# Optimization experiments

Measured on AMD Instinct MI355X. Metric: run time of the kernel, lower is better.

The kernel has to match this reference:

```python
import jax, jax.numpy as jnp
import numpy as np

NUM_ORI = 16
DEGREE = 2
NUM_LAYERS = 2
LN_EPS = 1e-6


def ori_grid_s1(n):
    theta = jnp.linspace(0.0, 2.0 * jnp.pi, n + 1)[:-1]
    return jnp.stack([jnp.cos(theta), jnp.sin(theta)], axis=-1)  # (O, 2)


def poly_feats(z, degree):
    # PolynomialFeatures: [z, z*z outer, (z*z)*z outer ...] flattened
    feats = [z]
    p = z
    for _ in range(degree):
        p = (p[..., :, None] * z[..., None, :]).reshape(*z.shape[:-1], -1)
        feats.append(p)
    return jnp.concatenate(feats, axis=-1)


def basis_mlp(z, W1, b1, W2, b2):
    return jax.nn.gelu(jax.nn.gelu(z @ W1 + b1) @ W2 + b2)


def layer_norm(h, scale, bias):
    mu = h.mean(axis=-1, keepdims=True)
    var = ((h - mu) ** 2).mean(axis=-1, keepdims=True)
    return (h - mu) * jax.lax.rsqrt(var + LN_EPS) * scale + bias


def setup_inputs() -> dict:
    key = jax.random.key(0)
    ks = jax.random.split(key, 16)
    B, N, NIN, H, BD, WF, OUT, L = 1, 256, 3, 64, 32, 4, 3, NUM_LAYERS
    s = 0.05
    return {
        'pos': jax.random.normal(ks[0], (B, N, 2), jnp.float32),
        'x': jax.random.normal(ks[1], (B, N, NIN), jnp.float32),
        'skb_W1': jax.random.normal(ks[2], (14, H), jnp.float32) * s,
        'skb_b1': jnp.zeros((H,), jnp.float32),
        'skb_W2': jax.random.normal(ks[3], (H, BD), jnp.float32) * s,
        'skb_b2': jnp.zeros((BD,), jnp.float32),
        'rkb_W1': jax.random.normal(ks[4], (3, H), jnp.float32) * s,
        'rkb_b1': jnp.zeros((H,), jnp.float32),
        'rkb_W2': jax.random.normal(ks[5], (H, BD), jnp.float32) * s,
        'rkb_b2': jnp.zeros((BD,), jnp.float32),
        'emb_W': jax.random.normal(ks[6], (NIN, H), jnp.float32) * s,
        'conv_sW': jax.random.normal(ks[7], (L, BD, H), jnp.float32) * s,
        'conv_rW': jax.random.normal(ks[8], (L, BD, H), jnp.float32) * s,
        'conv_b': jnp.zeros((L, H), jnp.float32),
        'ln_scale': jnp.ones((L, H), jnp.float32),
        'ln_bias': jnp.zeros((L, H), jnp.float32),
        'lin1_W': jax.random.normal(ks[9], (L, H, WF * H), jnp.float32) * s,
        'lin1_b': jnp.zeros((L, WF * H), jnp.float32),
        'lin2_W': jax.random.normal(ks[10], (L, WF * H, H), jnp.float32) * s,
        'lin2_b': jnp.zeros((L, H), jnp.float32),
        'readout_W': jax.random.normal(ks[11], (H, OUT), jnp.float32) * s,
    }


def reference(pos, x, skb_W1, skb_b1, skb_W2, skb_b2, rkb_W1, rkb_b1, rkb_W2, rkb_b2,
              emb_W, conv_sW, conv_rW, conv_b, ln_scale, ln_bias,
              lin1_W, lin1_b, lin2_W, lin2_b, readout_W):
    ori = ori_grid_s1(NUM_ORI)  # (O, 2)
    # rel_pos: (B, n, m, 1, 2) -> broadcast against ori (O, 2)
    rel_pos = pos[:, None, :, None, :] - pos[:, :, None, None, :]
    inv1 = jnp.sum(rel_pos * ori[None, None, None, :, :], axis=-1, keepdims=True)  # (B,N,N,O,1)
    inv2 = jnp.linalg.norm(rel_pos - rel_pos * inv1, axis=-1, keepdims=True)       # (B,N,N,O,1)
    spatial_inv = jnp.concatenate([inv1, inv2], axis=-1)                            # (B,N,N,O,2)
    orient_inv = jnp.sum(ori[:, None, :] * ori[None, :, :], axis=-1, keepdims=True) # (O,O,1)

    kernel_basis = basis_mlp(poly_feats(spatial_inv, DEGREE), skb_W1, skb_b1, skb_W2, skb_b2)  # (B,N,N,O,BD)
    fiber_basis = basis_mlp(poly_feats(orient_inv, DEGREE), rkb_W1, rkb_b1, rkb_W2, rkb_b2)    # (O,O,BD)

    h = x @ emb_W                                  # (B,N,H)
    O = NUM_ORI
    h = jnp.broadcast_to(h[:, :, None, :], (h.shape[0], h.shape[1], O, h.shape[2]))  # (B,N,O,H)

    for i in range(NUM_LAYERS):
        inp = h
        sk = kernel_basis @ conv_sW[i]             # (B,N,N,O,H)
        rk = fiber_basis @ conv_rW[i]              # (O,O,H)
        c = jnp.einsum('bnoc,bmnoc->bmoc', h, sk)  # spatial aggregation
        c = jnp.einsum('bmoc,poc->bmpc', c, rk)    # orientation mixing
        c = c + conv_b[i]
        c = layer_norm(c, ln_scale[i], ln_bias[i])
        c = jax.nn.gelu(c @ lin1_W[i] + lin1_b[i]) @ lin2_W[i] + lin2_b[i]
        h = inp + c

    readout = h @ readout_W                        # (B,N,O,OUT)
    out_scalar = readout.mean(axis=-2)             # (B,N,OUT)
    out_scalar = jnp.sum(out_scalar, axis=1) / out_scalar.shape[1]  # global pool -> (B,OUT)
    return out_scalar
```

## Files before the change

### kernel.cpp

```cpp
#include <hip/hip_runtime.h>
#include <math.h>

#define NPTS 256
#define NORI 16
#define CH   64
#define BD   32
#define HID  64
#define STEP16 0.39269908169872414f

typedef __bf16 bf16x8 __attribute__((ext_vector_type(8)));
typedef float  f32x4  __attribute__((ext_vector_type(4)));

#define MFMA16(a, b, cc) __builtin_amdgcn_mfma_f32_16x16x32_bf16(a, b, cc, 0, 0, 0)
#define GLOAD_LDS16(g, l) \
    __builtin_amdgcn_global_load_lds((const __attribute__((address_space(1))) unsigned int*)(g), \
                                     (__attribute__((address_space(3))) unsigned int*)(l), 16, 0, 0)

__device__ __forceinline__ float gelu_f(float x) {
    float x2 = x * x;
    float y2 = x * fmaf(0.07135481627f, x2, 1.5957691216f);
    float e = __expf(y2);
    return x - x * __builtin_amdgcn_rcpf(e + 1.0f);
}

__device__ __forceinline__ unsigned pk2(float x, float y) {
    union { __bf16 h[2]; unsigned u; } r;
    r.h[0] = (__bf16)x; r.h[1] = (__bf16)y;
    return r.u;
}

__device__ __forceinline__ void dev_prep(
    const float* __restrict__ skb_W1, const float* __restrict__ skb_W2,
    const float* __restrict__ conv_sW,
    __bf16* __restrict__ w1T, __bf16* __restrict__ w2T, __bf16* __restrict__ w2Tlo,
    __bf16* __restrict__ sWT, __bf16* __restrict__ sWTlo, int t)
{
    if (t < 64) {
        float f[9];
        f[0] = skb_W1[t];
        f[1] = skb_W1[64 + t];
        f[2] = skb_W1[128 + t];
        f[3] = skb_W1[192 + t] + skb_W1[256 + t];
        f[4] = skb_W1[320 + t];
        f[5] = skb_W1[384 + t];
        f[6] = skb_W1[448 + t] + skb_W1[512 + t] + skb_W1[640 + t];
        f[7] = skb_W1[576 + t] + skb_W1[704 + t] + skb_W1[768 + t];
        f[8] = skb_W1[832 + t];
#pragma unroll
        for (int k = 0; k < 9; ++k) {
            __bf16 hi = (__bf16)f[k];
            w1T[t * 32 + k]      = hi;
            w1T[t * 32 + 9 + k]  = (__bf16)(f[k] - (float)hi);
            w1T[t * 32 + 18 + k] = hi;
        }
#pragma unroll
        for (int k = 27; k < 32; ++k) w1T[t * 32 + k] = (__bf16)0.0f;
    }
    for (int i = t; i < 2048; i += 256) {
        int n = i >> 6, kk = i & 63;
        float v = skb_W2[kk * 32 + n];
        __bf16 hi = (__bf16)v;
        w2T[i]   = hi;
        w2Tlo[i] = (__bf16)(v - (float)hi);
    }
    for (int i = t; i < 4096; i += 256) {
        int ll = i >> 11, chh = (i >> 5) & 63, k = i & 31;
        float v = conv_sW[(ll * 32 + k) * 64 + chh];
        __bf16 hi = (__bf16)v;
        sWT[i]   = hi;
        sWTlo[i] = (__bf16)(v - (float)hi);
    }
}

__device__ __forceinline__ void dev_fiber(
    const float* __restrict__ rkb_W1, const float* __restrict__ rkb_b1,
    const float* __restrict__ rkb_W2, const float* __restrict__ rkb_b2,
    const float* __restrict__ conv_rW, float* __restrict__ rk, int p, int t)
{
    __shared__ float w1L[3 * 64], b1L[64], w2L[64 * 32], b2L[32];
    __shared__ float rwL[2 * 32 * 64];
    __shared__ float t1L[16 * 64];
    __shared__ float fbL[16 * 32];

    if (t < 192) w1L[t] = rkb_W1[t];
    if (t >= 192 && t < 256) b1L[t - 192] = rkb_b1[t - 192];
    for (int i = t; i < 2048; i += 256) w2L[i] = rkb_W2[i];
    if (t < 32) b2L[t] = rkb_b2[t];
    for (int i = t; i < 4096; i += 256) rwL[i] = conv_rW[i];
    __syncthreads();

    const int o = t & 15;
    const float cp = cosf(p * STEP16), sp = sinf(p * STEP16);
    const float co = cosf(o * STEP16), so = sinf(o * STEP16);
    const float s0 = cp * co + sp * so;
    const float m1 = s0 * s0, m2 = m1 * s0;

    {
        const int jg = t >> 4;
#pragma unroll
        for (int u = 0; u < 4; ++u) {
            const int j = jg * 4 + u;
            float a = b1L[j] + s0 * w1L[j] + m1 * w1L[64 + j] + m2 * w1L[128 + j];
            t1L[o * 64 + j] = gelu_f(a);
        }
    }
    __syncthreads();
    {
        const int kg = t >> 4;
#pragma unroll
        for (int kk = 0; kk < 2; ++kk) {
            const int k = kg + kk * 16;
            float a = b2L[k];
#pragma unroll
            for (int j = 0; j < 64; ++j) a += t1L[o * 64 + j] * w2L[j * 32 + k];
            fbL[o * 32 + k] = gelu_f(a);
        }
    }
    __syncthreads();
    {
        const int o2 = t >> 4;
        const int chg = (t & 15) * 4;
#pragma unroll
        for (int l = 0; l < 2; ++l) {
            f32x4 acc = {0.f, 0.f, 0.f, 0.f};
#pragma unroll
            for (int k = 0; k < 32; ++k) {
                const float fv = fbL[o2 * 32 + k];
                const f32x4 rv = *(const f32x4*)(rwL + (l * 32 + k) * 64 + chg);
                acc[0] = fmaf(fv, rv[0], acc[0]);
                acc[1] = fmaf(fv, rv[1], acc[1]);
                acc[2] = fmaf(fv, rv[2], acc[2]);
                acc[3] = fmaf(fv, rv[3], acc[3]);
            }
            *(f32x4*)(rk + (l * 256 + p * 16 + o2) * 64 + chg) = acc;
        }
    }
}

__global__ __launch_bounds__(256) void k_prep(
    const float* __restrict__ skb_W1, const float* __restrict__ skb_W2,
    const float* __restrict__ conv_sW,
    __bf16* __restrict__ w1T, __bf16* __restrict__ w2T, __bf16* __restrict__ w2Tlo,
    __bf16* __restrict__ sWT, __bf16* __restrict__ sWTlo)
{
    dev_prep(skb_W1, skb_W2, conv_sW, w1T, w2T, w2Tlo, sWT, sWTlo, threadIdx.x);
}

__global__ __launch_bounds__(256) void k_fiber2(
    const float* __restrict__ rkb_W1, const float* __restrict__ rkb_b1,
    const float* __restrict__ rkb_W2, const float* __restrict__ rkb_b2,
    const float* __restrict__ conv_rW, float* __restrict__ rk)
{
    dev_fiber(rkb_W1, rkb_b1, rkb_W2, rkb_b2, conv_rW, rk, blockIdx.x, threadIdx.x);
}

__global__ __launch_bounds__(256) void k_init(
    const float* __restrict__ x, const float* __restrict__ emb_W, float* __restrict__ h)
{
    int idx = blockIdx.x * 256 + threadIdx.x;
    int ch = idx & 63;
    int n  = idx >> 10;
    h[idx] = x[n * 3] * emb_W[ch] + x[n * 3 + 1] * emb_W[64 + ch] + x[n * 3 + 2] * emb_W[128 + ch];
}

__global__ __launch_bounds__(256) void k_setup(
    const float* __restrict__ x, const float* __restrict__ emb_W, float* __restrict__ h2,
    const float* __restrict__ rkb_W1, const float* __restrict__ rkb_b1,
    const float* __restrict__ rkb_W2, const float* __restrict__ rkb_b2,
    const float* __restrict__ conv_rW, float* __restrict__ rk,
    const float* __restrict__ skb_W1, const float* __restrict__ skb_W2,
    const float* __restrict__ conv_sW,
    __bf16* __restrict__ w1T, __bf16* __restrict__ w2T, __bf16* __restrict__ w2Tlo,
    __bf16* __restrict__ sWT, __bf16* __restrict__ sWTlo)
{
    const int b = blockIdx.x, t = threadIdx.x;
    if (b < 1024) {
        int idx = b * 256 + t;
        int ch = (idx >> 4) & 63;
        int n  = idx >> 10;
        h2[idx] = x[n * 3] * emb_W[ch] + x[n * 3 + 1] * emb_W[64 + ch]
                + x[n * 3 + 2] * emb_W[128 + ch];
    } else if (b < 1040) {
        dev_fiber(rkb_W1, rkb_b1, rkb_W2, rkb_b2, conv_rW, rk, b - 1024, t);
    } else {
        dev_prep(skb_W1, skb_W2, conv_sW, w1T, w2T, w2Tlo, sWT, sWTlo, t);
    }
}

__global__ __launch_bounds__(256) void k_kb2(
    const float* __restrict__ pos,
    const float* __restrict__ skb_b1, const float* __restrict__ skb_b2,
    const __bf16* __restrict__ w1T, const __bf16* __restrict__ w2T,
    const __bf16* __restrict__ w2Tlo, __bf16* __restrict__ kb_g)
{
    const int t = threadIdx.x;
    const int c = t & 15, qq = (t >> 4) & 3, w = t >> 6;
    const int b = blockIdx.x;
    const int pair = b >> 2;
    const int ohalf = (b >> 1) & 1;
    const int mhalf = b & 1;
    const int m0 = (pair >> 4) * 16, n0 = (pair & 15) * 16;

    bf16x8 w1B[4], w2A[2][2], w2Alo[2][2];
    float b1x[4][4], b2x[2][4];
#pragma unroll
    for (int ni = 0; ni < 4; ++ni) {
        w1B[ni] = *(const bf16x8*)(w1T + (ni * 16 + c) * 32 + qq * 8);
#pragma unroll
        for (int r = 0; r < 4; ++r) b1x[ni][r] = skb_b1[ni * 16 + qq * 4 + r];
    }
#pragma unroll
    for (int mk = 0; mk < 2; ++mk) {
#pragma unroll
        for (int ks = 0; ks < 2; ++ks) {
            w2A[mk][ks]   = *(const bf16x8*)(w2T   + (mk * 16 + c) * 64 + ks * 32 + qq * 8);
            w2Alo[mk][ks] = *(const bf16x8*)(w2Tlo + (mk * 16 + c) * 64 + ks * 32 + qq * 8);
        }
#pragma unroll
        for (int r = 0; r < 4; ++r) b2x[mk][r] = skb_b2[mk * 16 + qq * 4 + r];
    }

    const int n = n0 + c;
    const float pnx = pos[2 * n], pny = pos[2 * n + 1];
    float cosv[4], sinv[4];
#pragma unroll
    for (int oi = 0; oi < 4; ++oi) {
        float th = (float)(ohalf * 4 + oi) * STEP16;
        cosv[oi] = cosf(th); sinv[oi] = sinf(th);
    }
    const int s0lane = c + ((qq & 1) << 5);
    const int s1lane = s0lane + 16;
    const int selhi = qq >> 1;
    const f32x4 zf = {0.f, 0.f, 0.f, 0.f};

#pragma unroll 1
    for (int mi2 = 0; mi2 < 2; ++mi2) {
        const int m = m0 + w * 4 + mhalf * 2 + mi2;
        const float dx = pnx - pos[2 * m];
        const float dy = pny - pos[2 * m + 1];
#pragma unroll
        for (int oi = 0; oi < 4; ++oi) {
            const int o = ohalf * 4 + oi;
            float a = dx * cosv[oi] + dy * sinv[oi];
            float vx = dx - dx * a, vy = dy - dy * a;
            float b2 = sqrtf(vx * vx + vy * vy);
            float mfv[9];
            mfv[0] = a; mfv[1] = b2; mfv[2] = a * a; mfv[3] = a * b2; mfv[4] = b2 * b2;
            mfv[5] = mfv[2] * a; mfv[6] = mfv[2] * b2; mfv[7] = mfv[3] * b2; mfv[8] = mfv[4] * b2;
            __bf16 mh[9], ml[9];
#pragma unroll
            for (int i = 0; i < 9; ++i) {
                mh[i] = (__bf16)mfv[i];
                ml[i] = (__bf16)(mfv[i] - (float)mh[i]);
            }
            bf16x8 mb;
            if (qq == 0) {
                mb[0]=mh[0]; mb[1]=mh[1]; mb[2]=mh[2]; mb[3]=mh[3];
                mb[4]=mh[4]; mb[5]=mh[5]; mb[6]=mh[6]; mb[7]=mh[7];
            } else if (qq == 1) {
                mb[0]=mh[8]; mb[1]=mh[0]; mb[2]=mh[1]; mb[3]=mh[2];
                mb[4]=mh[3]; mb[5]=mh[4]; mb[6]=mh[5]; mb[7]=mh[6];
            } else if (qq == 2) {
                mb[0]=mh[7]; mb[1]=mh[8]; mb[2]=ml[0]; mb[3]=ml[1];
                mb[4]=ml[2]; mb[5]=ml[3]; mb[6]=ml[4]; mb[7]=ml[5];
            } else {
                mb[0]=ml[6]; mb[1]=ml[7]; mb[2]=ml[8]; mb[3]=(__bf16)0.0f;
                mb[4]=(__bf16)0.0f; mb[5]=(__bf16)0.0f; mb[6]=(__bf16)0.0f; mb[7]=(__bf16)0.0f;
            }

            unsigned t1p[4][2];
#pragma unroll
            for (int ni = 0; ni < 4; ++ni) {
                f32x4 acc = MFMA16(w1B[ni], mb, zf);
                float g0 = gelu_f(acc[0] + b1x[ni][0]);
                float g1 = gelu_f(acc[1] + b1x[ni][1]);
                float g2 = gelu_f(acc[2] + b1x[ni][2]);
                float g3 = gelu_f(acc[3] + b1x[ni][3]);
                t1p[ni][0] = pk2(g0, g1);
                t1p[ni][1] = pk2(g2, g3);
            }

            bf16x8 B2[2];
#pragma unroll
            for (int ks = 0; ks < 2; ++ks) {
                const unsigned lo0 = t1p[ks * 2][0],     lo1 = t1p[ks * 2][1];
                const unsigned hi0 = t1p[ks * 2 + 1][0], hi1 = t1p[ks * 2 + 1][1];
                unsigned aL0 = (unsigned)__shfl((int)lo0, s0lane);
                unsigned aL1 = (unsigned)__shfl((int)lo1, s0lane);
                unsigned aL2 = (unsigned)__shfl((int)lo0, s1lane);
                unsigned aL3 = (unsigned)__shfl((int)lo1, s1lane);
                unsigned aH0 = (unsigned)__shfl((int)hi0, s0lane);
                unsigned aH1 = (unsigned)__shfl((int)hi1, s0lane);
                unsigned aH2 = (unsigned)__shfl((int)hi0, s1lane);
                unsigned aH3 = (unsigned)__shfl((int)hi1, s1lane);
                union { unsigned u[4]; bf16x8 v; } bu;
                bu.u[0] = selhi ? aH0 : aL0;
                bu.u[1] = selhi ? aH1 : aL1;
                bu.u[2] = selhi ? aH2 : aL2;
                bu.u[3] = selhi ? aH3 : aL3;
                B2[ks] = bu.v;
            }

            const size_t ptP = (size_t)((m * 256 + n) * 16 + o);
            const size_t ptM = (size_t)((n * 256 + m) * 16 + (o ^ 8));
            const int swz = o & 3;
#pragma unroll
            for (int mk = 0; mk < 2; ++mk) {
                f32x4 acc = MFMA16(w2A[mk][0], B2[0], zf);
                acc = MFMA16(w2A[mk][1], B2[1], acc);
                acc = MFMA16(w2Alo[mk][0], B2[0], acc);
                acc = MFMA16(w2Alo[mk][1], B2[1], acc);
                float g0 = gelu_f(acc[0] + b2x[mk][0]);
                float g1 = gelu_f(acc[1] + b2x[mk][1]);
                float g2 = gelu_f(acc[2] + b2x[mk][2]);
                float g3 = gelu_f(acc[3] + b2x[mk][3]);
                uint2 pv; pv.x = pk2(g0, g1); pv.y = pk2(g2, g3);
                const int off = (((mk * 2 + (qq >> 1)) ^ swz) << 4) + ((qq & 1) << 3);
                *(uint2*)((char*)kb_g + ptP * 64 + off) = pv;
                *(uint2*)((char*)kb_g + ptM * 64 + off) = pv;
            }
        }
    }
}

__global__ __launch_bounds__(1024) void k_conv3(
    const __bf16* __restrict__ kb_g,
    const __bf16* __restrict__ sWT, const __bf16* __restrict__ sWTlo,
    const float* __restrict__ conv_b, const float* __restrict__ rkg,
    const float* __restrict__ ln_scale, const float* __restrict__ ln_bias,
    const float* __restrict__ lin1_W, const float* __restrict__ lin1_b,
    const float* __restrict__ lin2_W, const float* __restrict__ lin2_b,
    const float* __restrict__ h_in, float* __restrict__ h_out, int l)
{
    __shared__ __align__(16) unsigned char smem[90112];
    const int t = threadIdx.x;
    const int m = blockIdx.x;
    const int w = t >> 6, lane = t & 63;
    const int qq = lane >> 4, c = lane & 15;
    const f32x4 zf = {0.f, 0.f, 0.f, 0.f};

    bf16x8 sWB[4], sWBlo[4];
#pragma unroll
    for (int ni = 0; ni < 4; ++ni) {
        sWB[ni]   = *(const bf16x8*)(sWT   + l * 2048 + (ni * 16 + c) * 32 + qq * 8);
        sWBlo[ni] = *(const bf16x8*)(sWTlo + l * 2048 + (ni * 16 + c) * 32 + qq * 8);
    }

    f32x4 cacc[4];
#pragma unroll
    for (int ni = 0; ni < 4; ++ni)
#pragma unroll
        for (int r = 0; r < 4; ++r) cacc[ni][r] = 0.f;

    const char* kbm = (const char*)kb_g + (size_t)m * 262144;
    const char* gsrc0 = kbm + w * 1024 + lane * 16;
    char* lbase = (char*)smem + w * 1024;

    GLOAD_LDS16(gsrc0, lbase);
    f32x4 hc0, hc1, hc2, hc3;
    {
        const float* hp = h_in + w * 1024 + c * 16 + qq * 4;
        hc0 = *(const f32x4*)(hp);
        hc1 = *(const f32x4*)(hp + 256);
        hc2 = *(const f32x4*)(hp + 512);
        hc3 = *(const f32x4*)(hp + 768);
    }
    __syncthreads();

#pragma unroll 2
    for (int tile = 0; tile < 16; ++tile) {
        const int bufoff = (tile & 1) << 14;
        if (tile < 15)
            GLOAD_LDS16(gsrc0 + (size_t)(tile + 1) * 16384, lbase + (bufoff ^ 16384));
        const int tn = (tile < 15) ? tile + 1 : 15;
        const float* hpn = h_in + (tn * 16 + w) * 1024 + c * 16 + qq * 4;
        f32x4 hn0 = *(const f32x4*)(hpn);
        f32x4 hn1 = *(const f32x4*)(hpn + 256);
        f32x4 hn2 = *(const f32x4*)(hpn + 512);
        f32x4 hn3 = *(const f32x4*)(hpn + 768);

        bf16x8 aF = *(const bf16x8*)(smem + bufoff + (w * 16 + c) * 64 + ((qq ^ (c & 3)) << 4));
        f32x4 g;
        g = MFMA16(aF, sWB[0], zf);
        g = MFMA16(aF, sWBlo[0], g);
#pragma unroll
        for (int r = 0; r < 4; ++r) cacc[0][r] = fmaf(g[r], hc0[r], cacc[0][r]);
        g = MFMA16(aF, sWB[1], zf);
        g = MFMA16(aF, sWBlo[1], g);
#pragma unroll
        for (int r = 0; r < 4; ++r) cacc[1][r] = fmaf(g[r], hc1[r], cacc[1][r]);
        g = MFMA16(aF, sWB[2], zf);
        g = MFMA16(aF, sWBlo[2], g);
#pragma unroll
        for (int r = 0; r < 4; ++r) cacc[2][r] = fmaf(g[r], hc2[r], cacc[2][r]);
        g = MFMA16(aF, sWB[3], zf);
        g = MFMA16(aF, sWBlo[3], g);
#pragma unroll
        for (int r = 0; r < 4; ++r) cacc[3][r] = fmaf(g[r], hc3[r], cacc[3][r]);

        __syncthreads();
        hc0 = hn0; hc1 = hn1; hc2 = hn2; hc3 = hn3;
    }

    {
        float* c1p = (float*)smem;
#pragma unroll
        for (int ni = 0; ni < 4; ++ni)
#pragma unroll
            for (int r = 0; r < 4; ++r)
                c1p[w * 1024 + (qq * 4 + r) * 64 + ni * 16 + c] = cacc[ni][r];
    }
    __syncthreads();
    {
        float* c1p = (float*)smem;
        float* c1r = (float*)(smem + 65536);
        float s = 0.f;
#pragma unroll
        for (int ww = 0; ww < 16; ++ww) s += c1p[ww * 1024 + t];
        c1r[t] = s;
    }
    __syncthreads();

    {
        float* c1r = (float*)(smem + 65536);
        float* cns = (float*)(smem + 69632);
        const int ch = lane;
        const float cb  = conv_b[l * 64 + ch];
        const float lsc = ln_scale[l * 64 + ch], lbi = ln_bias[l * 64 + ch];
        const float* rkp = rkg + (l * 256 + w * 16) * 64 + ch;
        float s = cb;
#pragma unroll
        for (int o = 0; o < 16; ++o) s += c1r[o * 64 + ch] * rkp[o * 64];
        float red = s;
#pragma unroll
        for (int off = 32; off > 0; off >>= 1) red += __shfl_xor(red, off);
        float mu = red * (1.0f / 64.0f);
        float d = s - mu;
        float r2 = d * d;
#pragma unroll
        for (int off = 32; off > 0; off >>= 1) r2 += __shfl_xor(r2, off);
        cns[w * 64 + ch] = d * rsqrtf(r2 * (1.0f / 64.0f) + 1e-6f) * lsc + lbi;
    }
    __syncthreads();

    {
        float* cns = (float*)(smem + 69632);
        float* usS = (float*)(smem + 73728);
        const int j = t & 255, q4 = t >> 8;
        const float* W1l = lin1_W + l * 64 * 256;
        const float bl1 = lin1_b[l * 256 + j];
        float ua[4];
#pragma unroll
        for (int pi = 0; pi < 4; ++pi) ua[pi] = bl1;
#pragma unroll 4
        for (int c2 = 0; c2 < 64; ++c2) {
            const float wv = W1l[c2 * 256 + j];
#pragma unroll
            for (int pi = 0; pi < 4; ++pi)
                ua[pi] = fmaf(cns[(q4 * 4 + pi) * 64 + c2], wv, ua[pi]);
        }
#pragma unroll
        for (int pi = 0; pi < 4; ++pi) usS[(q4 * 4 + pi) * 256 + j] = gelu_f(ua[pi]);
    }
    __syncthreads();

    {
        float* usS = (float*)(smem + 73728);
        const int ch2 = t & 63, pg = t >> 6;
        const float* W2l = lin2_W + l * 256 * 64;
        float o0 = lin2_b[l * 64 + ch2];
#pragma unroll 4
        for (int j = 0; j < 256; ++j)
            o0 = fmaf(usS[pg * 256 + j], W2l[j * 64 + ch2], o0);
        const int i0 = m * 1024 + ch2 * 16 + pg;
        h_out[i0] = h_in[i0] + o0;
    }
}

__global__ __launch_bounds__(512, 1) void k_layer2(
    const float* __restrict__ pos,
    const float* __restrict__ skb_b1, const float* __restrict__ skb_b2,
    const __bf16* __restrict__ w1T, const __bf16* __restrict__ w2T,
    const __bf16* __restrict__ w2Tlo,
    const __bf16* __restrict__ sWT, const __bf16* __restrict__ sWTlo,
    const float* __restrict__ conv_b, const float* __restrict__ rkg,
    const float* __restrict__ ln_scale, const float* __restrict__ ln_bias,
    const float* __restrict__ lin1_W, const float* __restrict__ lin1_b,
    const float* __restrict__ lin2_W, const float* __restrict__ lin2_b,
    const float* __restrict__ h_in, float* __restrict__ h_out, int l)
{
    __shared__ __align__(16) unsigned char smem[57344];
    const int t = threadIdx.x;
    const int m = blockIdx.x;
    const int w = t >> 6, lane = t & 63;
    const int qq = lane >> 4, c = lane & 15;

    bf16x8 w1B[4], sWB[4], sWBlo[4], w2B[2][2], w2Blo[2][2];
    float b1v[4], b2v[2];
#pragma unroll
    for (int ni = 0; ni < 4; ++ni) {
        w1B[ni]   = *(const bf16x8*)(w1T + (ni * 16 + c) * 32 + qq * 8);
        sWB[ni]   = *(const bf16x8*)(sWT   + l * 2048 + (ni * 16 + c) * 32 + qq * 8);
        sWBlo[ni] = *(const bf16x8*)(sWTlo + l * 2048 + (ni * 16 + c) * 32 + qq * 8);
        b1v[ni] = skb_b1[ni * 16 + c];
    }
#pragma unroll
    for (int nt = 0; nt < 2; ++nt) {
        b2v[nt] = skb_b2[nt * 16 + c];
#pragma unroll
        for (int ks = 0; ks < 2; ++ks) {
            w2B[nt][ks]   = *(const bf16x8*)(w2T   + (nt * 16 + c) * 64 + ks * 32 + qq * 8);
            w2Blo[nt][ks] = *(const bf16x8*)(w2Tlo + (nt * 16 + c) * 64 + ks * 32 + qq * 8);
        }
    }

    const float pmx = pos[2 * m], pmy = pos[2 * m + 1];
    float co_ = 0.f, so_ = 0.f;
    if (t < 256) { float th = (float)(t & 15) * STEP16; co_ = cosf(th); so_ = sinf(th); }

    f32x4 cacc[4];
#pragma unroll
    for (int ni = 0; ni < 4; ++ni)
#pragma unroll
        for (int r = 0; r < 4; ++r) cacc[ni][r] = 0.f;

#pragma unroll 1
    for (int tile = 0; tile < 16; ++tile) {
        if (t < 256) {
            const int n = tile * 16 + (t >> 4);
            float dx = pos[2 * n] - pmx, dy = pos[2 * n + 1] - pmy;
            float a = dx * co_ + dy * so_;
            float vx = dx - dx * a, vy = dy - dy * a;
            float b = sqrtf(vx * vx + vy * vy);
            float mf[9];
            mf[0] = a; mf[1] = b; mf[2] = a * a; mf[3] = a * b; mf[4] = b * b;
            mf[5] = mf[2] * a; mf[6] = mf[2] * b; mf[7] = mf[3] * b; mf[8] = mf[4] * b;
            __bf16 s[32];
#pragma unroll
            for (int i = 0; i < 9; ++i) {
                __bf16 hi = (__bf16)mf[i];
                s[i] = hi; s[9 + i] = hi;
                s[18 + i] = (__bf16)(mf[i] - (float)hi);
            }
#pragma unroll
            for (int i = 27; i < 32; ++i) s[i] = (__bf16)0.0f;
            unsigned char* rowp = smem + t * 64;
#pragma unroll
            for (int u = 0; u < 4; ++u) {
                bf16x8 vv;
#pragma unroll
                for (int j = 0; j < 8; ++j) vv[j] = s[u * 8 + j];
                *(bf16x8*)(rowp + ((u ^ (t & 3)) << 4)) = vv;
            }
        }
        __syncthreads();

#pragma unroll
        for (int mm = 0; mm < 2; ++mm) {
            const int row = (2 * w + mm) * 16 + c;
            bf16x8 aF = *(const bf16x8*)(smem + row * 64 + ((qq ^ (row & 3)) << 4));
#pragma unroll
            for (int ni = 0; ni < 4; ++ni) {
                f32x4 acc = {0.f, 0.f, 0.f, 0.f};
                acc = MFMA16(aF, w1B[ni], acc);
#pragma unroll
                for (int r = 0; r < 4; ++r) {
                    const int ro = (2 * w + mm) * 16 + qq * 4 + r;
                    float g = gelu_f(acc[r] + b1v[ni]);
                    const int chc = ni * 16 + c;
                    *(__bf16*)(smem + 16384 + ro * 128 + (((chc >> 3) ^ (ro & 7)) << 4)
                               + ((chc & 7) << 1)) = (__bf16)g;
                }
            }
        }
        __syncthreads();

#pragma unroll
        for (int mm = 0; mm < 2; ++mm) {
            const int row = (2 * w + mm) * 16 + c;
            bf16x8 a0 = *(const bf16x8*)(smem + 16384 + row * 128 + ((qq ^ (row & 7)) << 4));
            bf16x8 a1 = *(const bf16x8*)(smem + 16384 + row * 128 + (((4 + qq) ^ (row & 7)) << 4));
#pragma unroll
            for (int nt = 0; nt < 2; ++nt) {
                f32x4 acc = {0.f, 0.f, 0.f, 0.f};
                acc = MFMA16(a0, w2B[nt][0], acc);
                acc = MFMA16(a1, w2B[nt][1], acc);
                acc = MFMA16(a0, w2Blo[nt][0], acc);
                acc = MFMA16(a1, w2Blo[nt][1], acc);
#pragma unroll
                for (int r = 0; r < 4; ++r) {
                    const int ro = (2 * w + mm) * 16 + qq * 4 + r;
                    float g = gelu_f(acc[r] + b2v[nt]);
                    const int kc = nt * 16 + c;
                    *(__bf16*)(smem + ro * 64 + (((kc >> 3) ^ (ro & 3)) << 4)
                               + ((kc & 7) << 1)) = (__bf16)g;
                }
            }
        }
        __syncthreads();

#pragma unroll
        for (int mm = 0; mm < 2; ++mm) {
            const int mi = 2 * w + mm;
            const int row = mi * 16 + c;
            bf16x8 aF = *(const bf16x8*)(smem + row * 64 + ((qq ^ (row & 3)) << 4));
            const int nbase = (tile * 16 + mi) * 1024 + qq * 256;
#pragma unroll
            for (int ni = 0; ni < 4; ++ni) {
                f32x4 g3 = {0.f, 0.f, 0.f, 0.f};
                g3 = MFMA16(aF, sWB[ni], g3);
                g3 = MFMA16(aF, sWBlo[ni], g3);
#pragma unroll
                for (int r = 0; r < 4; ++r) {
                    float hv = h_in[nbase + r * 64 + ni * 16 + c];
                    cacc[ni][r] = fmaf(g3[r], hv, cacc[ni][r]);
                }
            }
        }
        __syncthreads();
    }

    {
        float* c1p = (float*)smem;
#pragma unroll
        for (int ni = 0; ni < 4; ++ni)
#pragma unroll
            for (int r = 0; r < 4; ++r)
                c1p[w * 1024 + (qq * 4 + r) * 64 + ni * 16 + c] = cacc[ni][r];
    }
    __syncthreads();
    {
        float* c1p = (float*)smem;
        float* c1r = (float*)(smem + 32768);
        for (int i = t; i < 1024; i += 512) {
            float s = 0.f;
#pragma unroll
            for (int ww = 0; ww < 8; ++ww) s += c1p[ww * 1024 + i];
            c1r[i] = s;
        }
    }
    __syncthreads();

    {
        float* c1r = (float*)(smem + 32768);
        float* cns = (float*)(smem + 36864);
        const int ch = lane;
        const float cb  = conv_b[l * 64 + ch];
        const float lsc = ln_scale[l * 64 + ch], lbi = ln_bias[l * 64 + ch];
#pragma unroll
        for (int pp = 0; pp < 2; ++pp) {
            const int p = w + pp * 8;
            const float* rkp = rkg + (l * 256 + p * 16) * 64 + ch;
            float s = cb;
#pragma unroll
            for (int o = 0; o < 16; ++o) s += c1r[o * 64 + ch] * rkp[o * 64];
            float red = s;
#pragma unroll
            for (int off = 32; off > 0; off >>= 1) red += __shfl_xor(red, off);
            float mu = red * (1.0f / 64.0f);
            float d = s - mu;
            float r2 = d * d;
#pragma unroll
            for (int off = 32; off > 0; off >>= 1) r2 += __shfl_xor(r2, off);
            cns[p * 64 + ch] = d * rsqrtf(r2 * (1.0f / 64.0f) + 1e-6f) * lsc + lbi;
        }
    }
    __syncthreads();

    {
        float* cns = (float*)(smem + 36864);
        float* usS = (float*)(smem + 40960);
        const int j = t & 255, half = t >> 8;
        const float* W1l = lin1_W + l * 64 * 256;
        const float bl1 = lin1_b[l * 256 + j];
        float ua[8];
#pragma unroll
        for (int pi = 0; pi < 8; ++pi) ua[pi] = bl1;
#pragma unroll 1
        for (int c2 = 0; c2 < 64; ++c2) {
            const float wv = W1l[c2 * 256 + j];
#pragma unroll
            for (int pi = 0; pi < 8; ++pi)
                ua[pi] = fmaf(cns[(half * 8 + pi) * 64 + c2], wv, ua[pi]);
        }
#pragma unroll
        for (int pi = 0; pi < 8; ++pi) usS[(half * 8 + pi) * 256 + j] = gelu_f(ua[pi]);
    }
    __syncthreads();

    {
        float* usS = (float*)(smem + 40960);
        const int ch2 = t & 63, pg = t >> 6;
        const float* W2l = lin2_W + l * 256 * 64;
        const float bl2 = lin2_b[l * 64 + ch2];
        float o0 = bl2, o1 = bl2;
#pragma unroll 2
        for (int j = 0; j < 256; ++j) {
            const float wv = W2l[j * 64 + ch2];
            o0 = fmaf(usS[pg * 256 + j], wv, o0);
            o1 = fmaf(usS[(pg + 8) * 256 + j], wv, o1);
        }
        const int i0 = (m * 16 + pg) * 64 + ch2;
        const int i1 = (m * 16 + pg + 8) * 64 + ch2;
        h_out[i0] = h_in[i0] + o0;
        h_out[i1] = h_in[i1] + o1;
    }
}

__global__ __launch_bounds__(256) void k_readout_part(
    const float* __restrict__ h, float* __restrict__ part16)
{
    __shared__ float part[4][64];
    const int t = threadIdx.x, b = blockIdx.x;
    const int c = t & 63, seg = t >> 6;
    float s = 0.f;
    const int r0 = b * 256 + seg * 64;
    for (int r = r0; r < r0 + 64; ++r) s += h[r * 64 + c];
    part[seg][c] = s;
    __syncthreads();
    if (t < 64) part16[b * 64 + t] = part[0][t] + part[1][t] + part[2][t] + part[3][t];
}

__global__ __launch_bounds__(256) void k_readout_part2(
    const float* __restrict__ h, float* __restrict__ part16)
{
    const int t = threadIdx.x, b = blockIdx.x;
    const int ch = t >> 2, oq = t & 3;
    float s = 0.f;
#pragma unroll
    for (int nn = 0; nn < 16; ++nn) {
        const int n = b * 16 + nn;
        f32x4 v = *(const f32x4*)(h + n * 1024 + ch * 16 + oq * 4);
        s += (v[0] + v[1]) + (v[2] + v[3]);
    }
    s += __shfl_xor(s, 1);
    s += __shfl_xor(s, 2);
    if (oq == 0) part16[b * 64 + ch] = s;
}

__global__ __launch_bounds__(64) void k_readout_final(
    const float* __restrict__ part16, const float* __restrict__ rW, float* __restrict__ out)
{
    __shared__ float hbar[64];
    const int t = threadIdx.x;
    float s = 0.f;
#pragma unroll
    for (int b = 0; b < 16; ++b) s += part16[b * 64 + t];
    hbar[t] = s * (1.0f / 4096.0f);
    __syncthreads();
    if (t < 3) {
        float s2 = 0.f;
#pragma unroll
        for (int k = 0; k < 64; ++k) s2 += hbar[k] * rW[k * 3 + t];
        out[t] = s2;
    }
}

extern "C" void kernel_launch(void* const* d_in, const int* in_sizes, int n_in,
                              void* d_out, int out_size, void* d_ws, size_t ws_size,
                              hipStream_t stream)
{
    const float* pos      = (const float*)d_in[0];
    const float* x        = (const float*)d_in[1];
    const float* skb_W1   = (const float*)d_in[2];
    const float* skb_b1   = (const float*)d_in[3];
    const float* skb_W2   = (const float*)d_in[4];
    const float* skb_b2   = (const float*)d_in[5];
    const float* rkb_W1   = (const float*)d_in[6];
    const float* rkb_b1   = (const float*)d_in[7];
    const float* rkb_W2   = (const float*)d_in[8];
    const float* rkb_b2   = (const float*)d_in[9];
    const float* emb_W    = (const float*)d_in[10];
    const float* conv_sW  = (const float*)d_in[11];
    const float* conv_rW  = (const float*)d_in[12];
    const float* conv_b   = (const float*)d_in[13];
    const float* ln_scale = (const float*)d_in[14];
    const float* ln_bias  = (const float*)d_in[15];
    const float* lin1_W   = (const float*)d_in[16];
    const float* lin1_b   = (const float*)d_in[17];
    const float* lin2_W   = (const float*)d_in[18];
    const float* lin2_b   = (const float*)d_in[19];
    const float* readout_W= (const float*)d_in[20];
    float* out = (float*)d_out;

    unsigned char* ws = (unsigned char*)d_ws;
    float*  h_a    = (float*)(ws);
    float*  h_b    = (float*)(ws + 1048576);
    float*  rkw    = (float*)(ws + 2097152);
    __bf16* w1T    = (__bf16*)(ws + 2228224);
    __bf16* w2T    = (__bf16*)(ws + 2232320);
    __bf16* w2Tlo  = (__bf16*)(ws + 2236416);
    __bf16* sWT    = (__bf16*)(ws + 2240512);
    __bf16* sWTlo  = (__bf16*)(ws + 2248704);
    float*  part16 = (float*)(ws + 2256896);
    __bf16* kb_g   = (__bf16*)(ws + 2260992);

    const bool fast = (ws_size >= 2260992ull + 67108864ull);

    if (fast) {
        k_setup<<<1041, 256, 0, stream>>>(x, emb_W, h_a,
                                          rkb_W1, rkb_b1, rkb_W2, rkb_b2, conv_rW, rkw,
                                          skb_W1, skb_W2, conv_sW,
                                          w1T, w2T, w2Tlo, sWT, sWTlo);
        k_kb2<<<1024, 256, 0, stream>>>(pos, skb_b1, skb_b2, w1T, w2T, w2Tlo, kb_g);
        k_conv3<<<256, 1024, 0, stream>>>(kb_g, sWT, sWTlo, conv_b, rkw,
                                          ln_scale, ln_bias, lin1_W, lin1_b,
                                          lin2_W, lin2_b, h_a, h_b, 0);
        k_conv3<<<256, 1024, 0, stream>>>(kb_g, sWT, sWTlo, conv_b, rkw,
                                          ln_scale, ln_bias, lin1_W, lin1_b,
                                          lin2_W, lin2_b, h_b, h_a, 1);
        k_readout_part2<<<16, 256, 0, stream>>>(h_a, part16);
        k_readout_final<<<1, 64, 0, stream>>>(part16, readout_W, out);
    } else {
        k_prep<<<1, 256, 0, stream>>>(skb_W1, skb_W2, conv_sW, w1T, w2T, w2Tlo, sWT, sWTlo);
        k_fiber2<<<16, 256, 0, stream>>>(rkb_W1, rkb_b1, rkb_W2, rkb_b2, conv_rW, rkw);
        k_init<<<1024, 256, 0, stream>>>(x, emb_W, h_a);
        k_layer2<<<256, 512, 0, stream>>>(pos, skb_b1, skb_b2, w1T, w2T, w2Tlo, sWT, sWTlo,
                                          conv_b, rkw, ln_scale, ln_bias, lin1_W, lin1_b,
                                          lin2_W, lin2_b, h_a, h_b, 0);
        k_layer2<<<256, 512, 0, stream>>>(pos, skb_b1, skb_b2, w1T, w2T, w2Tlo, sWT, sWTlo,
                                          conv_b, rkw, ln_scale, ln_bias, lin1_W, lin1_b,
                                          lin2_W, lin2_b, h_b, h_a, 1);
        k_readout_part<<<16, 256, 0, stream>>>(h_a, part16);
        k_readout_final<<<1, 64, 0, stream>>>(part16, readout_W, out);
    }
}
```

Before: 157.2 us.

## Replace per-tile block barriers with per-wave vmcnt waits in conv kernel

Each wave in the spatial-aggregation loop now reads only the LDS rows it loaded itself. The per-tile __syncthreads is therefore replaced by explicit s_waitcnt vmcnt counts that wait on the wave's own global-to-LDS loads. The last tile is peeled out of the loop, unrolling is dropped, and the direct-to-LDS loads get a nontemporal cache hint. This removes 16 block-wide barriers per kernel, but correctness now depends on the hand-counted vmcnt values matching the compiler's emitted loads.

```diff
diff --git a/kernel.cpp b/kernel.cpp
--- a/kernel.cpp
+++ b/kernel.cpp
@@ -12,9 +12,9 @@
 typedef float  f32x4  __attribute__((ext_vector_type(4)));
 
 #define MFMA16(a, b, cc) __builtin_amdgcn_mfma_f32_16x16x32_bf16(a, b, cc, 0, 0, 0)
-#define GLOAD_LDS16(g, l) \
+#define GLOAD_LDS16NT(g, l) \
     __builtin_amdgcn_global_load_lds((const __attribute__((address_space(1))) unsigned int*)(g), \
-                                     (__attribute__((address_space(3))) unsigned int*)(l), 16, 0, 0)
+                                     (__attribute__((address_space(3))) unsigned int*)(l), 16, 0, 2)
 
 __device__ __forceinline__ float gelu_f(float x) {
     float x2 = x * x;
@@ -323,7 +323,7 @@
     }
 }
 
-__global__ __launch_bounds__(1024) void k_conv3(
+__global__ __launch_bounds__(1024) void k_conv4(
     const __bf16* __restrict__ kb_g,
     const __bf16* __restrict__ sWT, const __bf16* __restrict__ sWTlo,
     const float* __restrict__ conv_b, const float* __restrict__ rkg,
@@ -355,8 +355,9 @@
     const char* kbm = (const char*)kb_g + (size_t)m * 262144;
     const char* gsrc0 = kbm + w * 1024 + lane * 16;
     char* lbase = (char*)smem + w * 1024;
-
-    GLOAD_LDS16(gsrc0, lbase);
+    const int myrow = (w * 16 + c) * 64 + ((qq ^ (c & 3)) << 4);
+
+    GLOAD_LDS16NT(gsrc0, lbase);
     f32x4 hc0, hc1, hc2, hc3;
     {
         const float* hp = h_in + w * 1024 + c * 16 + qq * 4;
@@ -365,21 +366,21 @@
         hc2 = *(const f32x4*)(hp + 512);
         hc3 = *(const f32x4*)(hp + 768);
     }
-    __syncthreads();
-
-#pragma unroll 2
-    for (int tile = 0; tile < 16; ++tile) {
+
+#pragma unroll 1
+    for (int tile = 0; tile < 15; ++tile) {
         const int bufoff = (tile & 1) << 14;
-        if (tile < 15)
-            GLOAD_LDS16(gsrc0 + (size_t)(tile + 1) * 16384, lbase + (bufoff ^ 16384));
-        const int tn = (tile < 15) ? tile + 1 : 15;
-        const float* hpn = h_in + (tn * 16 + w) * 1024 + c * 16 + qq * 4;
+        GLOAD_LDS16NT(gsrc0 + (size_t)(tile + 1) * 16384, lbase + (bufoff ^ 16384));
+        asm volatile("s_waitcnt vmcnt(5)" ::: "memory");
+        __builtin_amdgcn_sched_barrier(0);
+        bf16x8 aF = *(const bf16x8*)(smem + bufoff + myrow);
+
+        const float* hpn = h_in + ((tile + 1) * 16 + w) * 1024 + c * 16 + qq * 4;
         f32x4 hn0 = *(const f32x4*)(hpn);
         f32x4 hn1 = *(const f32x4*)(hpn + 256);
         f32x4 hn2 = *(const f32x4*)(hpn + 512);
         f32x4 hn3 = *(const f32x4*)(hpn + 768);
 
-        bf16x8 aF = *(const bf16x8*)(smem + bufoff + (w * 16 + c) * 64 + ((qq ^ (c & 3)) << 4));
         f32x4 g;
         g = MFMA16(aF, sWB[0], zf);
         g = MFMA16(aF, sWBlo[0], g);
@@ -398,9 +399,31 @@
 #pragma unroll
         for (int r = 0; r < 4; ++r) cacc[3][r] = fmaf(g[r], hc3[r], cacc[3][r]);
 
-        __syncthreads();
         hc0 = hn0; hc1 = hn1; hc2 = hn2; hc3 = hn3;
     }
+    {
+        asm volatile("s_waitcnt vmcnt(4)" ::: "memory");
+        __builtin_amdgcn_sched_barrier(0);
+        bf16x8 aF = *(const bf16x8*)(smem + ((15 & 1) << 14) + myrow);
+        f32x4 g;
+        g = MFMA16(aF, sWB[0], zf);
+        g = MFMA16(aF, sWBlo[0], g);
+#pragma unroll
+        for (int r = 0; r < 4; ++r) cacc[0][r] = fmaf(g[r], hc0[r], cacc[0][r]);
+        g = MFMA16(aF, sWB[1], zf);
+        g = MFMA16(aF, sWBlo[1], g);
+#pragma unroll
+        for (int r = 0; r < 4; ++r) cacc[1][r] = fmaf(g[r], hc1[r], cacc[1][r]);
+        g = MFMA16(aF, sWB[2], zf);
+        g = MFMA16(aF, sWBlo[2], g);
+#pragma unroll
+        for (int r = 0; r < 4; ++r) cacc[2][r] = fmaf(g[r], hc2[r], cacc[2][r]);
+        g = MFMA16(aF, sWB[3], zf);
+        g = MFMA16(aF, sWBlo[3], g);
+#pragma unroll
+        for (int r = 0; r < 4; ++r) cacc[3][r] = fmaf(g[r], hc3[r], cacc[3][r]);
+    }
+    __syncthreads();
 
     {
         float* c1p = (float*)smem;
@@ -803,10 +826,10 @@
                                           skb_W1, skb_W2, conv_sW,
                                           w1T, w2T, w2Tlo, sWT, sWTlo);
         k_kb2<<<1024, 256, 0, stream>>>(pos, skb_b1, skb_b2, w1T, w2T, w2Tlo, kb_g);
-        k_conv3<<<256, 1024, 0, stream>>>(kb_g, sWT, sWTlo, conv_b, rkw,
+        k_conv4<<<256, 1024, 0, stream>>>(kb_g, sWT, sWTlo, conv_b, rkw,
                                           ln_scale, ln_bias, lin1_W, lin1_b,
                                           lin2_W, lin2_b, h_a, h_b, 0);
-        k_conv3<<<256, 1024, 0, stream>>>(kb_g, sWT, sWTlo, conv_b, rkw,
+        k_conv4<<<256, 1024, 0, stream>>>(kb_g, sWT, sWTlo, conv_b, rkw,
                                           ln_scale, ln_bias, lin1_W, lin1_b,
                                           lin2_W, lin2_b, h_b, h_a, 1);
         k_readout_part2<<<16, 256, 0, stream>>>(h_a, part16);
```

After: 146.2 us. 1.08x faster.
